# Performance work log

Hardware: AMD Instinct MI355X
Metric: run time of the kernel (lower is better)

## Reference

```python
import jax, jax.numpy as jnp
import numpy as np

N, E, B = 50000, 800000, 512
DIN, H, A, BT = 128, 256, 40, 5


def _ln(h, g, b):
    m = jnp.mean(h, -1, keepdims=True)
    v = jnp.mean((h - m) ** 2, -1, keepdims=True)
    return (h - m) * jax.lax.rsqrt(v + 1e-5) * g + b


def _gcn(x, w, b, src, dst, n):
    # PyG GCNConv: add self-loops, symmetric D^-1/2 (A+I) D^-1/2 normalization
    h = x @ w
    loop = jnp.arange(n)
    s = jnp.concatenate([src, loop])
    d = jnp.concatenate([dst, loop])
    deg = jax.ops.segment_sum(jnp.ones(s.shape[0], h.dtype), d, num_segments=n)
    dinv = jax.lax.rsqrt(jnp.maximum(deg, 1.0))
    coef = (dinv[s] * dinv[d])[:, None]
    return jax.ops.segment_sum(coef * h[s], d, num_segments=n) + b


def _mlp2(x, w1, b1, w2, b2):
    return jax.nn.relu(x @ w1 + b1) @ w2 + b2


def _mlp3(x, w1, b1, w2, b2, w3, b3):
    h = jax.nn.relu(x @ w1 + b1)
    h = jax.nn.relu(h @ w2 + b2)
    return h @ w3 + b3


def setup_inputs() -> dict:
    key = jax.random.key(0)
    ks = iter(jax.random.split(key, 64))
    p = lambda shape: jax.random.normal(next(ks), shape, jnp.float32) * 0.05
    inp = {}
    inp["x"] = jax.random.normal(next(ks), (N, DIN), jnp.float32)
    inp["edge_index"] = jax.random.randint(next(ks), (2, E), 0, N)
    inp["batch"] = jnp.sort(jax.random.randint(next(ks), (N,), 0, B))
    inp["new_node_indices"] = jax.random.randint(next(ks), (B,), 0, N)
    inp["focus_node_indices"] = jax.random.randint(next(ks), (B,), 0, N)
    inp["num_graphs"] = B
    inp["conv_w0"] = p((DIN, H)); inp["conv_b0"] = p((H,))
    inp["conv_w1"] = p((H, H)); inp["conv_b1"] = p((H,))
    inp["conv_w2"] = p((H, H)); inp["conv_b2"] = p((H,))
    for i in range(3):
        inp[f"ln_g{i}"] = jnp.ones((H,), jnp.float32)
        inp[f"ln_b{i}"] = jnp.zeros((H,), jnp.float32)
    inp["res_w0"] = p((DIN, H)); inp["res_b0"] = p((H,))
    inp["stop_w1"] = p((H, H)); inp["stop_b1"] = p((H,))
    inp["stop_w2"] = p((H, 1)); inp["stop_b2"] = p((1,))
    inp["addn_w1"] = p((H, H)); inp["addn_b1"] = p((H,))
    inp["addn_w2"] = p((H, A)); inp["addn_b2"] = p((A,))
    inp["addb_w1"] = p((H, H)); inp["addb_b1"] = p((H,))
    inp["addb_w2"] = p((H, BT)); inp["addb_b2"] = p((BT,))
    inp["edge_w1"] = p((2 * H, H)); inp["edge_b1"] = p((H,))
    inp["edge_w2"] = p((H, H // 2)); inp["edge_b2"] = p((H // 2,))
    inp["edge_w3"] = p((H // 2, 1)); inp["edge_b3"] = p((1,))
    inp["bond_w1"] = p((2 * H, H)); inp["bond_b1"] = p((H,))
    inp["bond_w2"] = p((H, H // 2)); inp["bond_b2"] = p((H // 2,))
    inp["bond_w3"] = p((H // 2, BT)); inp["bond_b3"] = p((BT,))
    return inp


def reference(x, edge_index, batch, new_node_indices, focus_node_indices, num_graphs,
              conv_w0, conv_b0, conv_w1, conv_b1, conv_w2, conv_b2,
              ln_g0, ln_b0, ln_g1, ln_b1, ln_g2, ln_b2,
              res_w0, res_b0,
              stop_w1, stop_b1, stop_w2, stop_b2,
              addn_w1, addn_b1, addn_w2, addn_b2,
              addb_w1, addb_b1, addb_w2, addb_b2,
              edge_w1, edge_b1, edge_w2, edge_b2, edge_w3, edge_b3,
              bond_w1, bond_b1, bond_w2, bond_b2, bond_w3, bond_b3):
    n = x.shape[0]
    src, dst = edge_index[0], edge_index[1]
    conv_params = [(conv_w0, conv_b0), (conv_w1, conv_b1), (conv_w2, conv_b2)]
    ln_params = [(ln_g0, ln_b0), (ln_g1, ln_b1), (ln_g2, ln_b2)]
    h = x
    for i in range(3):
        h_in = h
        cw, cb = conv_params[i]
        lg, lb = ln_params[i]
        h = _gcn(h, cw, cb, src, dst, n)
        h = jax.nn.relu(_ln(h, lg, lb))  # dropout: eval mode (identity)
        res = h_in @ res_w0 + res_b0 if i == 0 else h_in
        h = h + res
    node_embeddings = h  # [N, H]
    # global mean pool over graphs
    counts = jax.ops.segment_sum(jnp.ones(n, h.dtype), batch, num_segments=num_graphs)
    graph_embedding = jax.ops.segment_sum(node_embeddings, batch, num_segments=num_graphs) / jnp.maximum(counts, 1.0)[:, None]
    stop_logits = _mlp2(graph_embedding, stop_w1, stop_b1, stop_w2, stop_b2)
    add_node_logits = _mlp2(graph_embedding, addn_w1, addn_b1, addn_w2, addn_b2)
    add_bond_logits = _mlp2(node_embeddings[focus_node_indices], addb_w1, addb_b1, addb_w2, addb_b2)
    # pair each node with its graph's newly added node
    new_node_embeddings = node_embeddings[new_node_indices]  # [B, H]
    pair = jnp.concatenate([node_embeddings, new_node_embeddings[batch]], axis=1)  # [N, 2H]
    edge_selection_logits = _mlp3(pair, edge_w1, edge_b1, edge_w2, edge_b2, edge_w3, edge_b3)
    bond_type_logits = _mlp3(pair, bond_w1, bond_b1, bond_w2, bond_b2, bond_w3, bond_b3)
    return (stop_logits, add_node_logits, add_bond_logits, node_embeddings,
            edge_selection_logits, bond_type_logits)
```

## Files before the change

### kernel.cpp

```cpp
#include <hip/hip_runtime.h>

typedef short bf16x8 __attribute__((ext_vector_type(8)));
typedef float f32x4 __attribute__((ext_vector_type(4)));
typedef unsigned short u16;
typedef u16 u16x4 __attribute__((ext_vector_type(4)));
typedef u16 u16x8 __attribute__((ext_vector_type(8)));

__device__ __forceinline__ float bf2f(u16 u) {
  union { float f; unsigned int i; } x; x.i = ((unsigned int)u) << 16; return x.f;
}
__device__ __forceinline__ u16 f2bf(float f) {
  union { float f; unsigned int i; } x; x.f = f;
  unsigned int r = x.i + 0x7fffu + ((x.i >> 16) & 1u);
  return (u16)(r >> 16);
}
__device__ __forceinline__ void st_out_(void* out, size_t idx, float v, int f32) {
  if (f32) ((float*)out)[idx] = v;
  else ((u16*)out)[idx] = f2bf(v);
}

__global__ void k_detect(const u16* __restrict__ xx, int* flag) {
  int j = threadIdx.x;
  u16 u = xx[2 * j];
  int ex = (u >> 7) & 0xFF;
  int insane = (u != 0) && (ex < 100 || ex > 140);
  unsigned long long m = __ballot(insane);
  if (j == 0) flag[0] = (__popcll(m) > 8) ? 1 : 0;
}

__global__ void k_cvt_big(const void* __restrict__ src, u16* __restrict__ dst, int n,
                          const int* __restrict__ flag) {
  int i = blockIdx.x * 256 + threadIdx.x;
  if (i >= n) return;
  dst[i] = (*flag) ? f2bf(((const float*)src)[i]) : ((const u16*)src)[i];
}

#define NSEG 38
struct Cvt { const void* src[NSEG]; int off[NSEG + 1]; };
__global__ void k_cvt_all(Cvt c, u16* __restrict__ dst, int total, const int* __restrict__ flag) {
  int i = blockIdx.x * 256 + threadIdx.x;
  if (i >= total) return;
  int s = 0;
  #pragma unroll 1
  while (i >= c.off[s + 1]) s++;
  int j = i - c.off[s];
  dst[i] = (*flag) ? f2bf(((const float*)c.src[s])[j]) : ((const u16*)c.src[s])[j];
}

struct Tr { const u16* src[8]; u16* dst[8]; int lk[8]; int nc[8]; int off[9]; };
__global__ void k_tr_all(Tr c, int total) {
  int i = blockIdx.x * 256 + threadIdx.x;
  if (i >= total) return;
  int s = 0;
  #pragma unroll 1
  while (i >= c.off[s + 1]) s++;
  int j = i - c.off[s];
  int K = 1 << c.lk[s];
  int nrow = j >> c.lk[s], k = j & (K - 1);
  c.dst[s][j] = c.src[s][k * c.nc[s] + nrow];
}

__global__ void k_init(int* deg, int* cursor, int n) {
  int i = blockIdx.x * 256 + threadIdx.x;
  if (i < n) { deg[i] = 1; cursor[i] = 0; }
}
__global__ void k_deg(const int* __restrict__ dst, int* deg, int e) {
  int i = blockIdx.x * 256 + threadIdx.x;
  if (i < e) atomicAdd(&deg[dst[i]], 1);
}
__global__ void k_dinv(const int* __restrict__ deg, float* dinv, int n) {
  int i = blockIdx.x * 256 + threadIdx.x;
  if (i < n) dinv[i] = rsqrtf((float)deg[i]);
}
#define SCB 4096
__global__ __launch_bounds__(256) void k_scanA(const int* __restrict__ deg, int* bsum, int n) {
  int b = blockIdx.x, t = threadIdx.x;
  int base = b * SCB;
  int s = 0;
  for (int j = t; j < SCB; j += 256) { int i = base + j; s += (i < n) ? deg[i] - 1 : 0; }
  int l = t & 63, wid = t >> 6;
  #pragma unroll
  for (int o = 32; o; o >>= 1) s += __shfl_xor(s, o);
  __shared__ int red[4];
  if (l == 0) red[wid] = s;
  __syncthreads();
  if (t == 0) bsum[b] = red[0] + red[1] + red[2] + red[3];
}
__global__ void k_scanB(int* bsum, int nb, int* off, int n) {
  if (threadIdx.x == 0) {
    int c = 0;
    for (int i = 0; i < nb; i++) { int v = bsum[i]; bsum[i] = c; c += v; }
    off[n] = c;
  }
}
__global__ __launch_bounds__(256) void k_scanC(const int* __restrict__ deg, const int* __restrict__ bsum,
                                               int* off, int n) {
  int b = blockIdx.x, t = threadIdx.x;
  int base = b * SCB + t * 16;
  int loc[16]; int s = 0;
  #pragma unroll
  for (int j = 0; j < 16; j++) { int i = base + j; loc[j] = s; s += (i < n) ? deg[i] - 1 : 0; }
  int l = t & 63, wid = t >> 6;
  int incl = s;
  #pragma unroll
  for (int o = 1; o < 64; o <<= 1) { int y = __shfl_up(incl, o); if (l >= o) incl += y; }
  int excl = incl - s;
  __shared__ int ws[4];
  if (l == 63) ws[wid] = incl;
  __syncthreads();
  int woff = 0;
  for (int w = 0; w < wid; w++) woff += ws[w];
  int pre = bsum[b] + woff + excl;
  #pragma unroll
  for (int j = 0; j < 16; j++) { int i = base + j; if (i < n) off[i] = pre + loc[j]; }
}
__global__ void k_csr(const int* __restrict__ src, const int* __restrict__ dst,
                      const int* __restrict__ off, int* cursor, int* csr_src, int e) {
  int i = blockIdx.x * 256 + threadIdx.x;
  if (i >= e) return;
  int d = dst[i], s = src[i];
  int slot = atomicAdd(&cursor[d], 1);
  csr_src[off[d] + slot] = s;
}

template <int EPI>
__global__ __launch_bounds__(256) void gemm_w(
    const u16* __restrict__ A, int lda,
    const u16* __restrict__ Bt,
    u16* __restrict__ C, int ldc,
    int M, int K, int NC,
    const u16* __restrict__ colbias,
    const float* __restrict__ rowbias, int rbld, const int* __restrict__ rowmap) {
  __shared__ u16 Bs[64 * 256];
  const int t = threadIdx.x;
  const int n0 = blockIdx.x * 64;
  const int m0 = blockIdx.y * 256;
  {
    const int ng = K >> 3;
    const int tot = 64 * ng;
    for (int i = t; i < tot; i += 256) {
      int c = i / ng, g = i - c * ng;
      u16x8 v = *reinterpret_cast<const u16x8*>(Bt + (size_t)(n0 + c) * K + g * 8);
      int gs = g ^ (c & 7);
      *reinterpret_cast<u16x8*>(&Bs[c * K + gs * 8]) = v;
    }
  }
  __syncthreads();

  const int wid = t >> 6, l = t & 63;
  const int rbase = m0 + wid * 64;
  const int lr = l & 15, lg = l >> 4;
  f32x4 acc[4][4] = {};
  const int nks = K >> 5;
  #pragma unroll 2
  for (int ks = 0; ks < nks; ks++) {
    bf16x8 af[4], bfr[4];
    #pragma unroll
    for (int mi = 0; mi < 4; mi++) {
      int row = rbase + mi * 16 + lr; if (row >= M) row = M - 1;
      af[mi] = *reinterpret_cast<const bf16x8*>(A + (size_t)row * lda + ks * 32 + lg * 8);
    }
    #pragma unroll
    for (int ni = 0; ni < 4; ni++) {
      int c = ni * 16 + lr;
      int g = (ks * 4 + lg) ^ (lr & 7);
      bfr[ni] = *reinterpret_cast<const bf16x8*>(&Bs[c * K + g * 8]);
    }
    #pragma unroll
    for (int mi = 0; mi < 4; mi++)
      #pragma unroll
      for (int ni = 0; ni < 4; ni++)
        acc[mi][ni] = __builtin_amdgcn_mfma_f32_16x16x32_bf16(af[mi], bfr[ni], acc[mi][ni], 0, 0, 0);
  }

  #pragma unroll
  for (int mi = 0; mi < 4; mi++) {
    int rowi[4];
    #pragma unroll
    for (int r = 0; r < 4; r++) rowi[r] = rbase + mi * 16 + lg * 4 + r;
    float rbv[4][4];
    if (EPI == 3) {
      int rmv[4];
      #pragma unroll
      for (int r = 0; r < 4; r++) {
        int rr = rowi[r]; if (rr >= M) rr = M - 1;
        rmv[r] = rowmap[rr];
      }
      #pragma unroll
      for (int ni = 0; ni < 4; ni++)
        #pragma unroll
        for (int r = 0; r < 4; r++)
          rbv[ni][r] = rowbias[(size_t)rmv[r] * rbld + n0 + ni * 16 + lr];
    }
    #pragma unroll
    for (int ni = 0; ni < 4; ni++) {
      int col = n0 + ni * 16 + lr;
      float cbv = 0.f;
      if (EPI == 1 || EPI == 2) cbv = bf2f(colbias[col]);
      #pragma unroll
      for (int r = 0; r < 4; r++) {
        if (rowi[r] < M) {
          float v = acc[mi][ni][r];
          if (EPI == 1 || EPI == 2) v += cbv;
          if (EPI == 3) v += rbv[ni][r];
          if (EPI == 2 || EPI == 3) v = fmaxf(v, 0.f);
          C[(size_t)rowi[r] * ldc + col] = f2bf(v);
        }
      }
    }
  }
}

__global__ __launch_bounds__(256, 6) void k_agg(
    const u16* __restrict__ hw, const u16* __restrict__ cb,
    const u16* __restrict__ lng, const u16* __restrict__ lnb,
    const u16* __restrict__ res, const float* __restrict__ dinv,
    const int* __restrict__ off, const int* __restrict__ csr_src,
    u16* __restrict__ hout, int n) {
  int l = threadIdx.x & 63;
  int v = blockIdx.x * 4 + (threadIdx.x >> 6);
  if (v >= n) return;
  const int half = l >> 5;
  const int c0 = (l & 31) * 8;
  float a[8] = {0, 0, 0, 0, 0, 0, 0, 0};
  int s = off[v], e = off[v + 1];
  int i = s;
  for (; i + 7 < e; i += 8) {
    int u0 = csr_src[i + half],     u1 = csr_src[i + 2 + half];
    int u2 = csr_src[i + 4 + half], u3 = csr_src[i + 6 + half];
    float w0 = dinv[u0], w1 = dinv[u1], w2 = dinv[u2], w3 = dinv[u3];
    u16x8 r0 = *reinterpret_cast<const u16x8*>(hw + (size_t)u0 * 256 + c0);
    u16x8 r1 = *reinterpret_cast<const u16x8*>(hw + (size_t)u1 * 256 + c0);
    u16x8 r2 = *reinterpret_cast<const u16x8*>(hw + (size_t)u2 * 256 + c0);
    u16x8 r3 = *reinterpret_cast<const u16x8*>(hw + (size_t)u3 * 256 + c0);
    #pragma unroll
    for (int j = 0; j < 8; j++)
      a[j] += w0 * bf2f(r0[j]) + w1 * bf2f(r1[j]) + w2 * bf2f(r2[j]) + w3 * bf2f(r3[j]);
  }
  for (; i < e; i += 2) {
    int idx = i + half;
    if (idx < e) {
      int u = csr_src[idx];
      float w = dinv[u];
      u16x8 r = *reinterpret_cast<const u16x8*>(hw + (size_t)u * 256 + c0);
      #pragma unroll
      for (int j = 0; j < 8; j++) a[j] += w * bf2f(r[j]);
    }
  }
  #pragma unroll
  for (int j = 0; j < 8; j++) a[j] += __shfl_xor(a[j], 32);
  float dv = dinv[v];
  u16x8 sv = *reinterpret_cast<const u16x8*>(hw + (size_t)v * 256 + c0);
  u16x8 cbv = *reinterpret_cast<const u16x8*>(cb + c0);
  float sum = 0.f;
  #pragma unroll
  for (int j = 0; j < 8; j++) {
    a[j] = dv * (dv * bf2f(sv[j]) + a[j]) + bf2f(cbv[j]);
    sum += a[j];
  }
  #pragma unroll
  for (int o = 16; o; o >>= 1) sum += __shfl_xor(sum, o);
  float mean = sum * (1.f / 256.f);
  float vs = 0.f;
  #pragma unroll
  for (int j = 0; j < 8; j++) { float d = a[j] - mean; vs += d * d; }
  #pragma unroll
  for (int o = 16; o; o >>= 1) vs += __shfl_xor(vs, o);
  float rs = rsqrtf(vs * (1.f / 256.f) + 1e-5f);
  u16x8 gv = *reinterpret_cast<const u16x8*>(lng + c0);
  u16x8 bv = *reinterpret_cast<const u16x8*>(lnb + c0);
  u16x8 rv = *reinterpret_cast<const u16x8*>(res + (size_t)v * 256 + c0);
  u16x8 ov;
  #pragma unroll
  for (int j = 0; j < 8; j++)
    ov[j] = f2bf(fmaxf((a[j] - mean) * rs * bf2f(gv[j]) + bf2f(bv[j]), 0.f) + bf2f(rv[j]));
  if (half == 0)
    *reinterpret_cast<u16x8*>(hout + (size_t)v * 256 + c0) = ov;
}

__global__ __launch_bounds__(256) void k_pool(const u16* __restrict__ h, const int* __restrict__ batch,
                                              int n, float* gemb) {
  int g = blockIdx.x, c = threadIdx.x;
  int lo = 0, hi = n;
  while (lo < hi) { int mid = (lo + hi) >> 1; if (batch[mid] < g) lo = mid + 1; else hi = mid; }
  int s = lo;
  lo = s; hi = n;
  while (lo < hi) { int mid = (lo + hi) >> 1; if (batch[mid] < g + 1) lo = mid + 1; else hi = mid; }
  int e = lo;
  float acc = 0.f;
  for (int i = s; i < e; i++) acc += bf2f(h[(size_t)i * 256 + c]);
  int cnt = e - s; if (cnt < 1) cnt = 1;
  gemb[g * 256 + c] = acc / (float)cnt;
}

__global__ __launch_bounds__(256) void k_glin(const u16* __restrict__ h, const int* __restrict__ nidx,
                                              const u16* __restrict__ W, const u16* __restrict__ b1,
                                              float* g1, int ld, int ofs) {
  int b = blockIdx.x, t = threadIdx.x;
  __shared__ float sin_[256];
  sin_[t] = bf2f(h[(size_t)nidx[b] * 256 + t]);
  __syncthreads();
  float acc = bf2f(b1[t]);
  #pragma unroll 8
  for (int k = 0; k < 256; k++) acc += sin_[k] * bf2f(W[k * 256 + t]);
  g1[(size_t)b * ld + ofs + t] = acc;
}

template <int OUTD>
__global__ __launch_bounds__(256) void k_mlp2(const float* __restrict__ inf32,
                                              const u16* __restrict__ inbf, const int* __restrict__ idx,
                                              const u16* __restrict__ W1, const u16* __restrict__ b1,
                                              const u16* __restrict__ W2, const u16* __restrict__ b2,
                                              void* __restrict__ out, size_t obase,
                                              const int* __restrict__ flag) {
  int b = blockIdx.x, t = threadIdx.x;
  __shared__ float sin_[256];
  __shared__ float sh[256];
  sin_[t] = inf32 ? inf32[b * 256 + t] : bf2f(inbf[(size_t)idx[b] * 256 + t]);
  __syncthreads();
  float acc = bf2f(b1[t]);
  #pragma unroll 8
  for (int k = 0; k < 256; k++) acc += sin_[k] * bf2f(W1[k * 256 + t]);
  sh[t] = fmaxf(acc, 0.f);
  __syncthreads();
  if (t < OUTD) {
    float a2 = bf2f(b2[t]);
    #pragma unroll 8
    for (int k = 0; k < 256; k++) a2 += sh[k] * bf2f(W2[k * OUTD + t]);
    st_out_(out, obase + (size_t)b * OUTD + t, a2, *flag);
  }
}

__global__ __launch_bounds__(256) void k_final(const u16* __restrict__ t2e, const u16* __restrict__ t2b,
                                               const u16* __restrict__ w3e, const u16* __restrict__ b3e,
                                               const u16* __restrict__ w3b, const u16* __restrict__ b3b,
                                               void* __restrict__ out, size_t oe, size_t ob, int M,
                                               const int* __restrict__ flag) {
  int r = blockIdx.x * 4 + (threadIdx.x >> 6);
  int l = threadIdx.x & 63;
  if (r >= M) return;
  float p[6] = {0, 0, 0, 0, 0, 0};
  #pragma unroll
  for (int j = 0; j < 2; j++) {
    int k = l * 2 + j;
    float te = bf2f(t2e[(size_t)r * 128 + k]);
    float tb = bf2f(t2b[(size_t)r * 128 + k]);
    p[0] += te * bf2f(w3e[k]);
    #pragma unroll
    for (int q = 0; q < 5; q++) p[1 + q] += tb * bf2f(w3b[k * 5 + q]);
  }
  #pragma unroll
  for (int q = 0; q < 6; q++)
    #pragma unroll
    for (int o = 32; o; o >>= 1) p[q] += __shfl_xor(p[q], o);
  if (l == 0) {
    int f32 = *flag;
    st_out_(out, oe + r, p[0] + bf2f(b3e[0]), f32);
    #pragma unroll
    for (int q = 0; q < 5; q++)
      st_out_(out, ob + (size_t)r * 5 + q, p[1 + q] + bf2f(b3b[q]), f32);
  }
}

__global__ void k_emit8(const u16* __restrict__ src, void* __restrict__ out, size_t obase, int n8,
                        const int* __restrict__ flag) {
  int i = blockIdx.x * 256 + threadIdx.x;
  if (i >= n8) return;
  u16x8 v = reinterpret_cast<const u16x8*>(src)[i];
  if (*flag) {
    float4* fo = (float4*)((float*)out + obase);
    float4 lo, hi;
    lo.x = bf2f(v[0]); lo.y = bf2f(v[1]); lo.z = bf2f(v[2]); lo.w = bf2f(v[3]);
    hi.x = bf2f(v[4]); hi.y = bf2f(v[5]); hi.z = bf2f(v[6]); hi.w = bf2f(v[7]);
    fo[(size_t)i * 2] = lo; fo[(size_t)i * 2 + 1] = hi;
  } else {
    reinterpret_cast<u16x8*>((u16*)out + obase)[i] = v;
  }
}

extern "C" void kernel_launch(void* const* d_in, const int* in_sizes, int n_in,
                              void* d_out, int out_size, void* d_ws, size_t ws_size,
                              hipStream_t stream) {
  const int N = in_sizes[0] / 128;
  const int E = in_sizes[1] / 2;
  const int B = in_sizes[3];

  const int* ei    = (const int*)d_in[1];
  const int* srcp  = ei;
  const int* dstp  = ei + E;
  const int* batch = (const int*)d_in[2];
  const int* newi  = (const int*)d_in[3];
  const int* focus = (const int*)d_in[4];

  const size_t o_stop = 0;
  const size_t o_addn = (size_t)B;
  const size_t o_addb = (size_t)B + (size_t)B * 40;
  const size_t o_emb  = o_addb + (size_t)B * 5;
  const size_t o_esel = o_emb + (size_t)N * 256;
  const size_t o_bond = o_esel + (size_t)N;

  char* p = (char*)d_ws;
  auto alloc = [&](size_t bytes) -> void* {
    void* r = (void*)p;
    p += (bytes + 255) & ~(size_t)255;
    return r;
  };
  int* flag = (int*)alloc(4);
  static const int seg_din[NSEG] = {6,7,8,9,10,11, 12,13,14,15,16,17, 18,19,
                                    20,21,22,23, 24,25,26,27, 28,29,30,31,
                                    32,33,34,35,36,37, 38,39,40,41,42,43};
  static const int seg_len[NSEG] = {32768,256,65536,256,65536,256, 256,256,256,256,256,256,
                                    32768,256, 65536,256,256,1, 65536,256,10240,40,
                                    65536,256,1280,5, 131072,256,32768,128,128,1,
                                    131072,256,32768,128,640,5};
  int wtotal = 0;
  int seg_off[NSEG + 1];
  for (int i = 0; i < NSEG; i++) { seg_off[i] = wtotal; wtotal += seg_len[i]; }
  seg_off[NSEG] = wtotal;
  u16* wbf = (u16*)alloc((size_t)wtotal * 2);
  u16* wt_cw0 = (u16*)alloc(256 * 128 * 2);
  u16* wt_cw1 = (u16*)alloc(256 * 256 * 2);
  u16* wt_cw2 = (u16*)alloc(256 * 256 * 2);
  u16* wt_res = (u16*)alloc(256 * 128 * 2);
  u16* wt_t1  = (u16*)alloc(512 * 256 * 2);
  u16* wt_e2  = (u16*)alloc(128 * 256 * 2);
  u16* wt_b2  = (u16*)alloc(128 * 256 * 2);
  int*   deg     = (int*)alloc((size_t)N * 4);
  int*   cursor  = (int*)alloc((size_t)N * 4);
  int*   off     = (int*)alloc((size_t)(N + 1) * 4);
  float* dinv    = (float*)alloc((size_t)N * 4);
  int*   bsum    = (int*)alloc(64 * 4);
  float* gemb    = (float*)alloc((size_t)B * 256 * 4);
  float* g1full  = (float*)alloc((size_t)B * 512 * 4);
  int*   csr_src = (int*)alloc((size_t)E * 4);
  u16*   xbf     = (u16*)alloc((size_t)N * 128 * 2);
  u16*   P1      = (u16*)alloc((size_t)N * 256 * 2);
  u16*   P2      = (u16*)alloc((size_t)N * 256 * 2);
  u16*   P3      = (u16*)alloc((size_t)N * 256 * 2);

  auto wseg = [&](int i) -> u16* { return wbf + seg_off[i]; };
  u16 *cw0 = wseg(0), *cb0 = wseg(1), *cw1 = wseg(2), *cb1 = wseg(3), *cw2 = wseg(4), *cb2 = wseg(5);
  u16 *lg0 = wseg(6), *lb0 = wseg(7), *lg1 = wseg(8), *lb1 = wseg(9), *lg2 = wseg(10), *lb2 = wseg(11);
  u16 *rw0 = wseg(12), *rb0 = wseg(13);
  u16 *sw1 = wseg(14), *sb1 = wseg(15), *sw2 = wseg(16), *sb2 = wseg(17);
  u16 *aw1 = wseg(18), *ab1 = wseg(19), *aw2 = wseg(20), *ab2 = wseg(21);
  u16 *bw1 = wseg(22), *bb1 = wseg(23), *bw2 = wseg(24), *bb2 = wseg(25);
  u16 *ew1 = wseg(26), *eb1 = wseg(27), *ew2 = wseg(28), *eb2 = wseg(29), *ew3 = wseg(30), *eb3 = wseg(31);
  u16 *qw1 = wseg(32), *qb1 = wseg(33), *qw2 = wseg(34), *qb2 = wseg(35), *qw3 = wseg(36), *qb3 = wseg(37);

  k_detect<<<1, 64, 0, stream>>>((const u16*)d_in[0], flag);
  k_cvt_big<<<(N * 128 + 255) / 256, 256, 0, stream>>>(d_in[0], xbf, N * 128, flag);
  Cvt cd;
  for (int i = 0; i < NSEG; i++) cd.src[i] = d_in[seg_din[i]];
  for (int i = 0; i <= NSEG; i++) cd.off[i] = seg_off[i];
  k_cvt_all<<<(wtotal + 255) / 256, 256, 0, stream>>>(cd, wbf, wtotal, flag);

  const int NB = (N + 255) / 256;
  const int EBk = (E + 255) / 256;
  const int NBS = (N + SCB - 1) / SCB;

  k_init<<<NB, 256, 0, stream>>>(deg, cursor, N);
  k_deg<<<EBk, 256, 0, stream>>>(dstp, deg, E);
  k_dinv<<<NB, 256, 0, stream>>>(deg, dinv, N);
  k_scanA<<<NBS, 256, 0, stream>>>(deg, bsum, N);
  k_scanB<<<1, 64, 0, stream>>>(bsum, NBS, off, N);
  k_scanC<<<NBS, 256, 0, stream>>>(deg, bsum, off, N);
  k_csr<<<EBk, 256, 0, stream>>>(srcp, dstp, off, cursor, csr_src, E);

  {
    Tr td;
    const u16* ts[8] = {cw0, cw1, cw2, rw0, ew1, qw1, ew2, qw2};
    u16* tdst[8] = {wt_cw0, wt_cw1, wt_cw2, wt_res, wt_t1, wt_t1 + 256 * 256, wt_e2, wt_b2};
    int tlk[8] = {7, 8, 8, 7, 8, 8, 8, 8};
    int tnc[8] = {256, 256, 256, 256, 256, 256, 128, 128};
    int tlen[8] = {32768, 65536, 65536, 32768, 65536, 65536, 32768, 32768};
    int tot = 0;
    for (int i = 0; i < 8; i++) {
      td.src[i] = ts[i]; td.dst[i] = tdst[i]; td.lk[i] = tlk[i]; td.nc[i] = tnc[i];
      td.off[i] = tot; tot += tlen[i];
    }
    td.off[8] = tot;
    k_tr_all<<<(tot + 255) / 256, 256, 0, stream>>>(td, tot);
  }

  const int MB = (N + 255) / 256;
  dim3 gw4(4, MB);
  dim3 gw8(8, MB);
  dim3 gw2(2, MB);
  const int AGB = (N + 3) / 4;

  gemm_w<1><<<gw4, 256, 0, stream>>>(xbf, 128, wt_res, P1, 256, N, 128, 256, rb0, nullptr, 0, nullptr);
  gemm_w<0><<<gw4, 256, 0, stream>>>(xbf, 128, wt_cw0, P2, 256, N, 128, 256, nullptr, nullptr, 0, nullptr);
  k_agg<<<AGB, 256, 0, stream>>>(P2, cb0, lg0, lb0, P1, dinv, off, csr_src, P3, N);
  gemm_w<0><<<gw4, 256, 0, stream>>>(P3, 256, wt_cw1, P2, 256, N, 256, 256, nullptr, nullptr, 0, nullptr);
  k_agg<<<AGB, 256, 0, stream>>>(P2, cb1, lg1, lb1, P3, dinv, off, csr_src, P1, N);
  gemm_w<0><<<gw4, 256, 0, stream>>>(P1, 256, wt_cw2, P2, 256, N, 256, 256, nullptr, nullptr, 0, nullptr);
  k_agg<<<AGB, 256, 0, stream>>>(P2, cb2, lg2, lb2, P1, dinv, off, csr_src, P3, N);

  k_emit8<<<(N * 256 / 8 + 255) / 256, 256, 0, stream>>>(P3, d_out, o_emb, N * 256 / 8, flag);

  k_pool<<<B, 256, 0, stream>>>(P3, batch, N, gemb);
  k_glin<<<B, 256, 0, stream>>>(P3, newi, ew1 + 256 * 256, eb1, g1full, 512, 0);
  k_glin<<<B, 256, 0, stream>>>(P3, newi, qw1 + 256 * 256, qb1, g1full, 512, 256);
  k_mlp2<1><<<B, 256, 0, stream>>>(gemb, nullptr, nullptr, sw1, sb1, sw2, sb2, d_out, o_stop, flag);
  k_mlp2<40><<<B, 256, 0, stream>>>(gemb, nullptr, nullptr, aw1, ab1, aw2, ab2, d_out, o_addn, flag);
  k_mlp2<5><<<B, 256, 0, stream>>>(nullptr, P3, focus, bw1, bb1, bw2, bb2, d_out, o_addb, flag);

  u16* T1 = P1;
  gemm_w<3><<<gw8, 256, 0, stream>>>(P3, 256, wt_t1, T1, 512, N, 256, 512, nullptr, g1full, 512, batch);
  u16* t2e = P3;
  u16* t2b = P3 + (size_t)N * 128;
  gemm_w<2><<<gw2, 256, 0, stream>>>(T1, 512, wt_e2, t2e, 128, N, 256, 128, eb2, nullptr, 0, nullptr);
  gemm_w<2><<<gw2, 256, 0, stream>>>(T1 + 256, 512, wt_b2, t2b, 128, N, 256, 128, qb2, nullptr, 0, nullptr);
  k_final<<<(N + 3) / 4, 256, 0, stream>>>(t2e, t2b, ew3, eb3, qw3, qb3, d_out, o_esel, o_bond, N, flag);
}
```

Before: 669.1 us.

## Stage A tiles via async global-to-LDS loads and fuse first-layer GEMMs

Rewrites the GEMM so the A operand is staged into double-buffered swizzled LDS through global_load_lds, with explicit vmcnt waits overlapping each load with MFMAs. K becomes a template parameter so LDS is sized to fit. The conv0 and residual projections are merged into one 512-wide GEMM with a zero-padded bias, and k_agg gains leading-dimension arguments to read the fused output. This removes a second pass over x and hides A-load latency, at the cost of extra LDS and hand-managed wait counts.

Measured after the change: 646.3 us. 1.04x faster.

```diff
diff --git a/kernel.cpp b/kernel.cpp
--- a/kernel.cpp
+++ b/kernel.cpp
@@ -3,7 +3,6 @@
 typedef short bf16x8 __attribute__((ext_vector_type(8)));
 typedef float f32x4 __attribute__((ext_vector_type(4)));
 typedef unsigned short u16;
-typedef u16 u16x4 __attribute__((ext_vector_type(4)));
 typedef u16 u16x8 __attribute__((ext_vector_type(8)));
 
 __device__ __forceinline__ float bf2f(u16 u) {
@@ -45,6 +44,11 @@
   while (i >= c.off[s + 1]) s++;
   int j = i - c.off[s];
   dst[i] = (*flag) ? f2bf(((const float*)c.src[s])[j]) : ((const u16*)c.src[s])[j];
+}
+
+__global__ void k_padbias(const u16* __restrict__ rb, u16* cbz) {
+  int i = blockIdx.x * 256 + threadIdx.x;
+  if (i < 512) cbz[i] = (i < 256) ? (u16)0 : rb[i - 256];
 }
 
 struct Tr { const u16* src[8]; u16* dst[8]; int lk[8]; int nc[8]; int off[9]; };
@@ -123,15 +127,16 @@
   csr_src[off[d] + slot] = s;
 }
 
-template <int EPI>
-__global__ __launch_bounds__(256) void gemm_w(
+template <int EPI, int K>
+__global__ __launch_bounds__(256) void gemm_p(
     const u16* __restrict__ A, int lda,
     const u16* __restrict__ Bt,
     u16* __restrict__ C, int ldc,
-    int M, int K, int NC,
+    int M, int NC,
     const u16* __restrict__ colbias,
     const float* __restrict__ rowbias, int rbld, const int* __restrict__ rowmap) {
-  __shared__ u16 Bs[64 * 256];
+  __shared__ u16 Bs[64 * K];
+  __shared__ u16 As[4 * 2 * 1024];
   const int t = threadIdx.x;
   const int n0 = blockIdx.x * 64;
   const int m0 = blockIdx.y * 256;
@@ -141,8 +146,7 @@
     for (int i = t; i < tot; i += 256) {
       int c = i / ng, g = i - c * ng;
       u16x8 v = *reinterpret_cast<const u16x8*>(Bt + (size_t)(n0 + c) * K + g * 8);
-      int gs = g ^ (c & 7);
-      *reinterpret_cast<u16x8*>(&Bs[c * K + gs * 8]) = v;
+      *reinterpret_cast<u16x8*>(&Bs[c * K + (g ^ (c & 7)) * 8]) = v;
     }
   }
   __syncthreads();
@@ -150,27 +154,54 @@
   const int wid = t >> 6, l = t & 63;
   const int rbase = m0 + wid * 64;
   const int lr = l & 15, lg = l >> 4;
+  u16* Aw = &As[wid * 2048];
+  const int jrow = l >> 3;
+  const int gsw = (l & 7) ^ (l >> 3);
+
+  auto stage = [&](int buf, int s) {
+    int mi = s & 3, kh = s >> 2;
+    u16* dst = Aw + buf * 1024;
+    #pragma unroll
+    for (int j = 0; j < 2; j++) {
+      int row = rbase + mi * 16 + j * 8 + jrow;
+      if (row >= M) row = M - 1;
+      __builtin_amdgcn_global_load_lds(
+          (const __attribute__((address_space(1))) unsigned int*)(A + (size_t)row * lda + kh * 64 + gsw * 8),
+          (__attribute__((address_space(3))) unsigned int*)(dst + j * 512), 16, 0, 0);
+    }
+  };
+
   f32x4 acc[4][4] = {};
-  const int nks = K >> 5;
-  #pragma unroll 2
-  for (int ks = 0; ks < nks; ks++) {
-    bf16x8 af[4], bfr[4];
-    #pragma unroll
-    for (int mi = 0; mi < 4; mi++) {
-      int row = rbase + mi * 16 + lr; if (row >= M) row = M - 1;
-      af[mi] = *reinterpret_cast<const bf16x8*>(A + (size_t)row * lda + ks * 32 + lg * 8);
-    }
-    #pragma unroll
-    for (int ni = 0; ni < 4; ni++) {
-      int c = ni * 16 + lr;
-      int g = (ks * 4 + lg) ^ (lr & 7);
-      bfr[ni] = *reinterpret_cast<const bf16x8*>(&Bs[c * K + g * 8]);
-    }
-    #pragma unroll
-    for (int mi = 0; mi < 4; mi++)
+  bf16x8 bfr[2][4];
+  const int S = (K >> 6) * 4;
+  stage(0, 0);
+  #pragma unroll
+  for (int s = 0; s < S; s++) {
+    const int buf = s & 1, mi = s & 3, kh = s >> 2;
+    if (s + 1 < S) {
+      stage(buf ^ 1, s + 1);
+      asm volatile("s_waitcnt vmcnt(2)" ::: "memory");
+    } else {
+      asm volatile("s_waitcnt vmcnt(0)" ::: "memory");
+    }
+    __builtin_amdgcn_sched_barrier(0);
+    if (mi == 0) {
+      #pragma unroll
+      for (int ks = 0; ks < 2; ks++)
+        #pragma unroll
+        for (int ni = 0; ni < 4; ni++) {
+          int g = kh * 8 + ks * 4 + lg;
+          bfr[ks][ni] = *reinterpret_cast<const bf16x8*>(&Bs[(ni * 16 + lr) * K + (g ^ (lr & 7)) * 8]);
+        }
+    }
+    const u16* Ab = Aw + buf * 1024;
+    #pragma unroll
+    for (int ks = 0; ks < 2; ks++) {
+      bf16x8 af = *reinterpret_cast<const bf16x8*>(&Ab[lr * 64 + ((ks * 4 + lg) ^ (lr & 7)) * 8]);
       #pragma unroll
       for (int ni = 0; ni < 4; ni++)
-        acc[mi][ni] = __builtin_amdgcn_mfma_f32_16x16x32_bf16(af[mi], bfr[ni], acc[mi][ni], 0, 0, 0);
+        acc[mi][ni] = __builtin_amdgcn_mfma_f32_16x16x32_bf16(af, bfr[ks][ni], acc[mi][ni], 0, 0, 0);
+    }
   }
 
   #pragma unroll
@@ -212,9 +243,9 @@
 }
 
 __global__ __launch_bounds__(256, 6) void k_agg(
-    const u16* __restrict__ hw, const u16* __restrict__ cb,
+    const u16* __restrict__ hw, int hwld, const u16* __restrict__ cb,
     const u16* __restrict__ lng, const u16* __restrict__ lnb,
-    const u16* __restrict__ res, const float* __restrict__ dinv,
+    const u16* __restrict__ res, int resld, const float* __restrict__ dinv,
     const int* __restrict__ off, const int* __restrict__ csr_src,
     u16* __restrict__ hout, int n) {
   int l = threadIdx.x & 63;
@@ -229,10 +260,10 @@
     int u0 = csr_src[i + half],     u1 = csr_src[i + 2 + half];
     int u2 = csr_src[i + 4 + half], u3 = csr_src[i + 6 + half];
     float w0 = dinv[u0], w1 = dinv[u1], w2 = dinv[u2], w3 = dinv[u3];
-    u16x8 r0 = *reinterpret_cast<const u16x8*>(hw + (size_t)u0 * 256 + c0);
-    u16x8 r1 = *reinterpret_cast<const u16x8*>(hw + (size_t)u1 * 256 + c0);
-    u16x8 r2 = *reinterpret_cast<const u16x8*>(hw + (size_t)u2 * 256 + c0);
-    u16x8 r3 = *reinterpret_cast<const u16x8*>(hw + (size_t)u3 * 256 + c0);
+    u16x8 r0 = *reinterpret_cast<const u16x8*>(hw + (size_t)u0 * hwld + c0);
+    u16x8 r1 = *reinterpret_cast<const u16x8*>(hw + (size_t)u1 * hwld + c0);
+    u16x8 r2 = *reinterpret_cast<const u16x8*>(hw + (size_t)u2 * hwld + c0);
+    u16x8 r3 = *reinterpret_cast<const u16x8*>(hw + (size_t)u3 * hwld + c0);
     #pragma unroll
     for (int j = 0; j < 8; j++)
       a[j] += w0 * bf2f(r0[j]) + w1 * bf2f(r1[j]) + w2 * bf2f(r2[j]) + w3 * bf2f(r3[j]);
@@ -242,7 +273,7 @@
     if (idx < e) {
       int u = csr_src[idx];
       float w = dinv[u];
-      u16x8 r = *reinterpret_cast<const u16x8*>(hw + (size_t)u * 256 + c0);
+      u16x8 r = *reinterpret_cast<const u16x8*>(hw + (size_t)u * hwld + c0);
       #pragma unroll
       for (int j = 0; j < 8; j++) a[j] += w * bf2f(r[j]);
     }
@@ -250,7 +281,7 @@
   #pragma unroll
   for (int j = 0; j < 8; j++) a[j] += __shfl_xor(a[j], 32);
   float dv = dinv[v];
-  u16x8 sv = *reinterpret_cast<const u16x8*>(hw + (size_t)v * 256 + c0);
+  u16x8 sv = *reinterpret_cast<const u16x8*>(hw + (size_t)v * hwld + c0);
   u16x8 cbv = *reinterpret_cast<const u16x8*>(cb + c0);
   float sum = 0.f;
   #pragma unroll
@@ -269,7 +300,7 @@
   float rs = rsqrtf(vs * (1.f / 256.f) + 1e-5f);
   u16x8 gv = *reinterpret_cast<const u16x8*>(lng + c0);
   u16x8 bv = *reinterpret_cast<const u16x8*>(lnb + c0);
-  u16x8 rv = *reinterpret_cast<const u16x8*>(res + (size_t)v * 256 + c0);
+  u16x8 rv = *reinterpret_cast<const u16x8*>(res + (size_t)v * resld + c0);
   u16x8 ov;
   #pragma unroll
   for (int j = 0; j < 8; j++)
@@ -418,13 +449,13 @@
   for (int i = 0; i < NSEG; i++) { seg_off[i] = wtotal; wtotal += seg_len[i]; }
   seg_off[NSEG] = wtotal;
   u16* wbf = (u16*)alloc((size_t)wtotal * 2);
-  u16* wt_cw0 = (u16*)alloc(256 * 128 * 2);
+  u16* wt_f0  = (u16*)alloc(512 * 128 * 2);
   u16* wt_cw1 = (u16*)alloc(256 * 256 * 2);
   u16* wt_cw2 = (u16*)alloc(256 * 256 * 2);
-  u16* wt_res = (u16*)alloc(256 * 128 * 2);
   u16* wt_t1  = (u16*)alloc(512 * 256 * 2);
   u16* wt_e2  = (u16*)alloc(128 * 256 * 2);
   u16* wt_b2  = (u16*)alloc(128 * 256 * 2);
+  u16* cbz    = (u16*)alloc(512 * 2);
   int*   deg     = (int*)alloc((size_t)N * 4);
   int*   cursor  = (int*)alloc((size_t)N * 4);
   int*   off     = (int*)alloc((size_t)(N + 1) * 4);
@@ -454,6 +485,7 @@
   for (int i = 0; i < NSEG; i++) cd.src[i] = d_in[seg_din[i]];
   for (int i = 0; i <= NSEG; i++) cd.off[i] = seg_off[i];
   k_cvt_all<<<(wtotal + 255) / 256, 256, 0, stream>>>(cd, wbf, wtotal, flag);
+  k_padbias<<<2, 256, 0, stream>>>(rb0, cbz);
 
   const int NB = (N + 255) / 256;
   const int EBk = (E + 255) / 256;
@@ -469,11 +501,11 @@
 
   {
     Tr td;
-    const u16* ts[8] = {cw0, cw1, cw2, rw0, ew1, qw1, ew2, qw2};
-    u16* tdst[8] = {wt_cw0, wt_cw1, wt_cw2, wt_res, wt_t1, wt_t1 + 256 * 256, wt_e2, wt_b2};
-    int tlk[8] = {7, 8, 8, 7, 8, 8, 8, 8};
+    const u16* ts[8] = {cw0, rw0, cw1, cw2, ew1, qw1, ew2, qw2};
+    u16* tdst[8] = {wt_f0, wt_f0 + 256 * 128, wt_cw1, wt_cw2, wt_t1, wt_t1 + 256 * 256, wt_e2, wt_b2};
+    int tlk[8] = {7, 7, 8, 8, 8, 8, 8, 8};
     int tnc[8] = {256, 256, 256, 256, 256, 256, 128, 128};
-    int tlen[8] = {32768, 65536, 65536, 32768, 65536, 65536, 32768, 32768};
+    int tlen[8] = {32768, 32768, 65536, 65536, 65536, 65536, 32768, 32768};
     int tot = 0;
     for (int i = 0; i < 8; i++) {
       td.src[i] = ts[i]; td.dst[i] = tdst[i]; td.lk[i] = tlk[i]; td.nc[i] = tnc[i];
@@ -484,18 +516,15 @@
   }
 
   const int MB = (N + 255) / 256;
-  dim3 gw4(4, MB);
-  dim3 gw8(8, MB);
-  dim3 gw2(2, MB);
   const int AGB = (N + 3) / 4;
-
-  gemm_w<1><<<gw4, 256, 0, stream>>>(xbf, 128, wt_res, P1, 256, N, 128, 256, rb0, nullptr, 0, nullptr);
-  gemm_w<0><<<gw4, 256, 0, stream>>>(xbf, 128, wt_cw0, P2, 256, N, 128, 256, nullptr, nullptr, 0, nullptr);
-  k_agg<<<AGB, 256, 0, stream>>>(P2, cb0, lg0, lb0, P1, dinv, off, csr_src, P3, N);
-  gemm_w<0><<<gw4, 256, 0, stream>>>(P3, 256, wt_cw1, P2, 256, N, 256, 256, nullptr, nullptr, 0, nullptr);
-  k_agg<<<AGB, 256, 0, stream>>>(P2, cb1, lg1, lb1, P3, dinv, off, csr_src, P1, N);
-  gemm_w<0><<<gw4, 256, 0, stream>>>(P1, 256, wt_cw2, P2, 256, N, 256, 256, nullptr, nullptr, 0, nullptr);
-  k_agg<<<AGB, 256, 0, stream>>>(P2, cb2, lg2, lb2, P1, dinv, off, csr_src, P3, N);
+  u16* PF = P1;
+
+  gemm_p<1, 128><<<dim3(8, MB), 256, 0, stream>>>(xbf, 128, wt_f0, PF, 512, N, 512, cbz, nullptr, 0, nullptr);
+  k_agg<<<AGB, 256, 0, stream>>>(PF, 512, cb0, lg0, lb0, PF + 256, 512, dinv, off, csr_src, P3, N);
+  gemm_p<0, 256><<<dim3(4, MB), 256, 0, stream>>>(P3, 256, wt_cw1, P1, 256, N, 256, nullptr, nullptr, 0, nullptr);
+  k_agg<<<AGB, 256, 0, stream>>>(P1, 256, cb1, lg1, lb1, P3, 256, dinv, off, csr_src, P2, N);
+  gemm_p<0, 256><<<dim3(4, MB), 256, 0, stream>>>(P2, 256, wt_cw2, P1, 256, N, 256, nullptr, nullptr, 0, nullptr);
+  k_agg<<<AGB, 256, 0, stream>>>(P1, 256, cb2, lg2, lb2, P2, 256, dinv, off, csr_src, P3, N);
 
   k_emit8<<<(N * 256 / 8 + 255) / 256, 256, 0, stream>>>(P3, d_out, o_emb, N * 256 / 8, flag);
 
@@ -506,11 +535,11 @@
   k_mlp2<40><<<B, 256, 0, stream>>>(gemb, nullptr, nullptr, aw1, ab1, aw2, ab2, d_out, o_addn, flag);
   k_mlp2<5><<<B, 256, 0, stream>>>(nullptr, P3, focus, bw1, bb1, bw2, bb2, d_out, o_addb, flag);
 
-  u16* T1 = P1;
-  gemm_w<3><<<gw8, 256, 0, stream>>>(P3, 256, wt_t1, T1, 512, N, 256, 512, nullptr, g1full, 512, batch);
+  u16* T1 = PF;
+  gemm_p<3, 256><<<dim3(8, MB), 256, 0, stream>>>(P3, 256, wt_t1, T1, 512, N, 512, nullptr, g1full, 512, batch);
   u16* t2e = P3;
   u16* t2b = P3 + (size_t)N * 128;
-  gemm_w<2><<<gw2, 256, 0, stream>>>(T1, 512, wt_e2, t2e, 128, N, 256, 128, eb2, nullptr, 0, nullptr);
-  gemm_w<2><<<gw2, 256, 0, stream>>>(T1 + 256, 512, wt_b2, t2b, 128, N, 256, 128, qb2, nullptr, 0, nullptr);
+  gemm_p<2, 256><<<dim3(2, MB), 256, 0, stream>>>(T1, 512, wt_e2, t2e, 128, N, 128, eb2, nullptr, 0, nullptr);
+  gemm_p<2, 256><<<dim3(2, MB), 256, 0, stream>>>(T1 + 256, 512, wt_b2, t2b, 128, N, 128, qb2, nullptr, 0, nullptr);
   k_final<<<(N + 3) / 4, 256, 0, stream>>>(t2e, t2b, ew3, eb3, qw3, qb3, d_out, o_esel, o_bond, N, flag);
 }
```
